# Kernel tuning notes

Hardware: AMD Instinct MI355X
Metric: run time of the kernel (lower is better)

## Reference

```python
import jax, jax.numpy as jnp
import numpy as np


def setup_inputs() -> dict:
    key = jax.random.key(0)
    k1, k2 = jax.random.split(key)
    N_rays, N_samples, NJ = 4096, 96, 24
    pts = jax.random.normal(k1, (N_rays, N_samples, 3), dtype=jnp.float32)
    skts = jax.random.normal(k2, (N_rays, NJ, 4, 4), dtype=jnp.float32)
    return {"pts": pts, "skts": skts}


def reference(pts, skts):
    # pts: [R, S, 3] -> homogeneous [R, S, 4]
    pts_h = jnp.concatenate([pts, jnp.ones(pts.shape[:-1] + (1,), dtype=pts.dtype)], axis=-1)
    # skts: [R, J, 4, 4]; fused equivalent of expand/transpose/matmul/permute:
    # out[r, s, j, a] = sum_b skts[r, j, a, b] * pts_h[r, s, b]
    out = jnp.einsum("rjab,rsb->rsja", skts, pts_h)
    return out[..., :3]
```

## Files before the change

### kernel.cpp

```cpp
#include <hip/hip_runtime.h>


constexpr int S_DIM = 96;
constexpr int J_DIM = 24;
constexpr int SKT_STRIDE = 17;
constexpr int BLOCK = 256;
constexpr int PAIRS = S_DIM * J_DIM;
constexpr int ITERS = PAIRS / BLOCK;

__global__ __launch_bounds__(BLOCK) void w2l_kernel(
    const float* __restrict__ pts,
    const float* __restrict__ skts,
    float* __restrict__ out) {

    const int r = blockIdx.x;
    const int tid = threadIdx.x;

    __shared__ float s_skt[J_DIM * SKT_STRIDE];
    __shared__ float s_pts[S_DIM * 3];

    const float* __restrict__ skt_g = skts + (size_t)r * (J_DIM * 16);
    const float* __restrict__ pts_g = pts  + (size_t)r * (S_DIM * 3);

    for (int i = tid; i < J_DIM * 16 + S_DIM * 3; i += BLOCK) {
        if (i < J_DIM * 16) {
            s_skt[(i >> 4) * SKT_STRIDE + (i & 15)] = skt_g[i];
        } else {
            int k = i - J_DIM * 16;
            s_pts[k] = pts_g[k];
        }
    }
    __syncthreads();

    float* __restrict__ out_r = out + (size_t)r * (PAIRS * 3);

    #pragma unroll
    for (int it = 0; it < ITERS; ++it) {
        const int p = tid + it * BLOCK;
        const int s = p / J_DIM;
        const int j = p - s * J_DIM;

        const float x = s_pts[s * 3 + 0];
        const float y = s_pts[s * 3 + 1];
        const float z = s_pts[s * 3 + 2];

        const float* __restrict__ b = &s_skt[j * SKT_STRIDE];
        const float o0 = fmaf(b[0], x, fmaf(b[1], y, fmaf(b[2],  z, b[3])));
        const float o1 = fmaf(b[4], x, fmaf(b[5], y, fmaf(b[6],  z, b[7])));
        const float o2 = fmaf(b[8], x, fmaf(b[9], y, fmaf(b[10], z, b[11])));

        *reinterpret_cast<float3*>(out_r + (size_t)p * 3) = make_float3(o0, o1, o2);
    }
}

extern "C" void kernel_launch(void* const* d_in, const int* in_sizes, int n_in,
                              void* d_out, int out_size, void* d_ws, size_t ws_size,
                              hipStream_t stream) {
    const float* pts  = (const float*)d_in[0];
    const float* skts = (const float*)d_in[1];
    float* out = (float*)d_out;

    const int R = in_sizes[0] / (S_DIM * 3);
    w2l_kernel<<<R, BLOCK, 0, stream>>>(pts, skts, out);
}
```

Measured before the change: 25.14 us.

## Process two rays per block with prefetched float4 loads into double-buffered LDS

Each block now handles two rays. While computing the first ray it prefetches the second ray's transforms and points into registers using float4 loads, then writes them into a second shared-memory buffer. This hides global load latency behind compute and stores, and uses vectorized loads in place of scalar ones. In exchange the grid is halved (2048 blocks), which reduces parallelism, and the launch assumes R is even.

```diff
diff --git a/kernel.cpp b/kernel.cpp
--- a/kernel.cpp
+++ b/kernel.cpp
@@ -3,53 +3,79 @@
 
 constexpr int S_DIM = 96;
 constexpr int J_DIM = 24;
-constexpr int SKT_STRIDE = 17;
+constexpr int STR   = 17;
 constexpr int BLOCK = 256;
 constexpr int PAIRS = S_DIM * J_DIM;
 constexpr int ITERS = PAIRS / BLOCK;
+constexpr int RPB   = 2;
+constexpr int SKT_F4 = J_DIM * 4;
+constexpr int PTS_F4 = S_DIM * 3 / 4;
+constexpr int TOT_F4 = SKT_F4 + PTS_F4;
 
 __global__ __launch_bounds__(BLOCK) void w2l_kernel(
     const float* __restrict__ pts,
     const float* __restrict__ skts,
     float* __restrict__ out) {
 
-    const int r = blockIdx.x;
     const int tid = threadIdx.x;
+    const int r0  = blockIdx.x * RPB;
 
-    __shared__ float s_skt[J_DIM * SKT_STRIDE];
-    __shared__ float s_pts[S_DIM * 3];
+    __shared__ float s_skt[RPB][J_DIM * STR];
+    __shared__ float s_pts[RPB][S_DIM * 3];
 
-    const float* __restrict__ skt_g = skts + (size_t)r * (J_DIM * 16);
-    const float* __restrict__ pts_g = pts  + (size_t)r * (S_DIM * 3);
+    auto load_ray = [&](int r, float4& v) {
+        if (tid < SKT_F4) {
+            v = reinterpret_cast<const float4*>(skts + (size_t)r * (J_DIM * 16))[tid];
+        } else if (tid < TOT_F4) {
+            v = reinterpret_cast<const float4*>(pts + (size_t)r * (S_DIM * 3))[tid - SKT_F4];
+        }
+    };
+    auto write_lds = [&](int buf, const float4& v) {
+        if (tid < SKT_F4) {
+            int row = tid >> 2, c = (tid & 3) * 4;
+            float* d = &s_skt[buf][row * STR + c];
+            d[0] = v.x; d[1] = v.y; d[2] = v.z; d[3] = v.w;
+        } else if (tid < TOT_F4) {
+            float* d = &s_pts[buf][(tid - SKT_F4) * 4];
+            d[0] = v.x; d[1] = v.y; d[2] = v.z; d[3] = v.w;
+        }
+    };
 
-    for (int i = tid; i < J_DIM * 16 + S_DIM * 3; i += BLOCK) {
-        if (i < J_DIM * 16) {
-            s_skt[(i >> 4) * SKT_STRIDE + (i & 15)] = skt_g[i];
-        } else {
-            int k = i - J_DIM * 16;
-            s_pts[k] = pts_g[k];
-        }
-    }
+    float4 v;
+    load_ray(r0, v);
+    write_lds(0, v);
     __syncthreads();
 
-    float* __restrict__ out_r = out + (size_t)r * (PAIRS * 3);
+    for (int rr = 0; rr < RPB; ++rr) {
+        float4 nv;
+        if (rr + 1 < RPB) load_ray(r0 + rr + 1, nv);
 
-    #pragma unroll
-    for (int it = 0; it < ITERS; ++it) {
-        const int p = tid + it * BLOCK;
-        const int s = p / J_DIM;
-        const int j = p - s * J_DIM;
+        float* __restrict__ out_r = out + (size_t)(r0 + rr) * (PAIRS * 3);
+        const float* __restrict__ sk = s_skt[rr];
+        const float* __restrict__ sp = s_pts[rr];
 
-        const float x = s_pts[s * 3 + 0];
-        const float y = s_pts[s * 3 + 1];
-        const float z = s_pts[s * 3 + 2];
+        #pragma unroll
+        for (int it = 0; it < ITERS; ++it) {
+            const int p = tid + it * BLOCK;
+            const int s = p / J_DIM;
+            const int j = p - s * J_DIM;
 
-        const float* __restrict__ b = &s_skt[j * SKT_STRIDE];
-        const float o0 = fmaf(b[0], x, fmaf(b[1], y, fmaf(b[2],  z, b[3])));
-        const float o1 = fmaf(b[4], x, fmaf(b[5], y, fmaf(b[6],  z, b[7])));
-        const float o2 = fmaf(b[8], x, fmaf(b[9], y, fmaf(b[10], z, b[11])));
+            const float x = sp[s * 3 + 0];
+            const float y = sp[s * 3 + 1];
+            const float z = sp[s * 3 + 2];
 
-        *reinterpret_cast<float3*>(out_r + (size_t)p * 3) = make_float3(o0, o1, o2);
+            const float* __restrict__ b = &sk[j * STR];
+            const float o0 = fmaf(b[0], x, fmaf(b[1], y, fmaf(b[2],  z, b[3])));
+            const float o1 = fmaf(b[4], x, fmaf(b[5], y, fmaf(b[6],  z, b[7])));
+            const float o2 = fmaf(b[8], x, fmaf(b[9], y, fmaf(b[10], z, b[11])));
+
+            *reinterpret_cast<float3*>(out_r + (size_t)p * 3) = make_float3(o0, o1, o2);
+        }
+
+        if (rr + 1 < RPB) {
+            write_lds(rr + 1, nv);
+            __syncthreads();
+        }
     }
 }
 
@@ -61,5 +87,5 @@
     float* out = (float*)d_out;
 
     const int R = in_sizes[0] / (S_DIM * 3);
-    w2l_kernel<<<R, BLOCK, 0, stream>>>(pts, skts, out);
+    w2l_kernel<<<R / RPB, BLOCK, 0, stream>>>(pts, skts, out);
 }
```

Result: faster. 23.92 us (-4.9%).

## Vectorize stores to float4, compute four joints per thread, two rays per block

Applied to the files above, without the earlier changes.

Each thread now computes 4 joints for one sample and writes 12 contiguous floats as three float4 stores, replacing the per-pair float3 stores. Shared memory holds points padded to float4 and skinning matrices at stride 20, so both are read with vector loads. Each 384-thread block processes two rays, which halves the grid size. The kernel is output-bandwidth bound, so the wider stores are meant to improve write efficiency, at the cost of a smaller grid and more registers per thread.

```diff
diff --git a/kernel.cpp b/kernel.cpp
--- a/kernel.cpp
+++ b/kernel.cpp
@@ -3,53 +3,76 @@
 
 constexpr int S_DIM = 96;
 constexpr int J_DIM = 24;
-constexpr int SKT_STRIDE = 17;
-constexpr int BLOCK = 256;
-constexpr int PAIRS = S_DIM * J_DIM;
-constexpr int ITERS = PAIRS / BLOCK;
+constexpr int BLOCK = 384;
+constexpr int RPB   = 2;
+constexpr int SKT_STR   = 20;
+constexpr int SKT_WORDS = J_DIM * SKT_STR;
+constexpr int PTS_WORDS = S_DIM * 4;
+constexpr int UNITS = RPB * S_DIM * J_DIM * 3 / 12;
+constexpr int ITERS = UNITS / BLOCK;
+constexpr int RAY_FLOATS = S_DIM * J_DIM * 3;
 
 __global__ __launch_bounds__(BLOCK) void w2l_kernel(
     const float* __restrict__ pts,
     const float* __restrict__ skts,
     float* __restrict__ out) {
 
-    const int r = blockIdx.x;
     const int tid = threadIdx.x;
+    const int r0  = blockIdx.x * RPB;
 
-    __shared__ float s_skt[J_DIM * SKT_STRIDE];
-    __shared__ float s_pts[S_DIM * 3];
+    __shared__ __align__(16) float s_skt[RPB][SKT_WORDS];
+    __shared__ __align__(16) float s_pts[RPB][PTS_WORDS];
 
-    const float* __restrict__ skt_g = skts + (size_t)r * (J_DIM * 16);
-    const float* __restrict__ pts_g = pts  + (size_t)r * (S_DIM * 3);
+    const float* __restrict__ skt_g = skts + (size_t)r0 * (J_DIM * 16);
+    const float* __restrict__ pts_g = pts  + (size_t)r0 * (S_DIM * 3);
 
-    for (int i = tid; i < J_DIM * 16 + S_DIM * 3; i += BLOCK) {
-        if (i < J_DIM * 16) {
-            s_skt[(i >> 4) * SKT_STRIDE + (i & 15)] = skt_g[i];
-        } else {
-            int k = i - J_DIM * 16;
-            s_pts[k] = pts_g[k];
-        }
+    if (tid < RPB * 96) {
+        float4 v = reinterpret_cast<const float4*>(skt_g)[tid];
+        int ray = tid / 96, g = tid - ray * 96;
+        int j = g >> 2, a = g & 3;
+        *reinterpret_cast<float4*>(&s_skt[ray][j * SKT_STR + a * 4]) = v;
+        int s = tid % S_DIM, ray2 = tid / S_DIM;
+        s_pts[ray2][s * 4 + 3] = 1.0f;
+    }
+    #pragma unroll
+    for (int q = tid; q < RPB * S_DIM * 3; q += BLOCK) {
+        float v = pts_g[q];
+        int ray = q / (S_DIM * 3), qq = q - ray * (S_DIM * 3);
+        int s = qq / 3, c = qq - s * 3;
+        s_pts[ray][s * 4 + c] = v;
     }
     __syncthreads();
 
-    float* __restrict__ out_r = out + (size_t)r * (PAIRS * 3);
+    float* __restrict__ out_p = out + (size_t)r0 * RAY_FLOATS;
 
     #pragma unroll
     for (int it = 0; it < ITERS; ++it) {
-        const int p = tid + it * BLOCK;
-        const int s = p / J_DIM;
-        const int j = p - s * J_DIM;
+        const int u   = tid + it * BLOCK;
+        const int ray = u / 576;
+        const int up  = u - ray * 576;
+        const int s   = up / 6;
+        const int jstart = (up - s * 6) * 4;
 
-        const float x = s_pts[s * 3 + 0];
-        const float y = s_pts[s * 3 + 1];
-        const float z = s_pts[s * 3 + 2];
+        const float4 P = *reinterpret_cast<const float4*>(&s_pts[ray][s * 4]);
+        const float* __restrict__ base = &s_skt[ray][jstart * SKT_STR];
 
-        const float* __restrict__ b = &s_skt[j * SKT_STRIDE];
-        const float o0 = fmaf(b[0], x, fmaf(b[1], y, fmaf(b[2],  z, b[3])));
-        const float o1 = fmaf(b[4], x, fmaf(b[5], y, fmaf(b[6],  z, b[7])));
-        const float o2 = fmaf(b[8], x, fmaf(b[9], y, fmaf(b[10], z, b[11])));
+        float o12[12];
+        #pragma unroll
+        for (int jj = 0; jj < 4; ++jj) {
+            const float4 B0 = *reinterpret_cast<const float4*>(base + jj * SKT_STR + 0);
+            const float4 B1 = *reinterpret_cast<const float4*>(base + jj * SKT_STR + 4);
+            const float4 B2 = *reinterpret_cast<const float4*>(base + jj * SKT_STR + 8);
+            o12[jj * 3 + 0] = fmaf(B0.x, P.x, fmaf(B0.y, P.y, fmaf(B0.z, P.z, B0.w)));
+            o12[jj * 3 + 1] = fmaf(B1.x, P.x, fmaf(B1.y, P.y, fmaf(B1.z, P.z, B1.w)));
+            o12[jj * 3 + 2] = fmaf(B2.x, P.x, fmaf(B2.y, P.y, fmaf(B2.z, P.z, B2.w)));
+        }
 
-        *reinterpret_cast<float3*>(out_r + (size_t)p * 3) = make_float3(o0, o1, o2);
+        float* __restrict__ dst = out_p + (size_t)u * 12;
+        #pragma unroll
+        for (int k = 0; k < 3; ++k) {
+            *reinterpret_cast<float4*>(dst + 4 * k) =
+                make_float4(o12[4 * k], o12[4 * k + 1], o12[4 * k + 2], o12[4 * k + 3]);
+        }
     }
 }
 
@@ -61,5 +84,5 @@
     float* out = (float*)d_out;
 
     const int R = in_sizes[0] / (S_DIM * 3);
-    w2l_kernel<<<R, BLOCK, 0, stream>>>(pts, skts, out);
+    w2l_kernel<<<R / RPB, BLOCK, 0, stream>>>(pts, skts, out);
 }
```

Measured after the change: 35.11 us. 39.7% more time.

## Process two rays per block with double-buffered LDS and register-held transforms

Applied to the files above, without the earlier changes.

Each block now handles two rays with 384 threads. Every thread keeps its joint's 3x4 transform in registers and reads padded float4 points from LDS. The next ray's inputs are prefetched into registers while the current ray computes, then written to the other LDS buffer. This cuts per-pair LDS loads and integer division, and overlaps global loads with compute. In exchange it halves the grid size, which may reduce latency hiding, and assumes R is even.

```diff
diff --git a/kernel.cpp b/kernel.cpp
--- a/kernel.cpp
+++ b/kernel.cpp
@@ -3,53 +3,80 @@
 
 constexpr int S_DIM = 96;
 constexpr int J_DIM = 24;
-constexpr int SKT_STRIDE = 17;
-constexpr int BLOCK = 256;
-constexpr int PAIRS = S_DIM * J_DIM;
-constexpr int ITERS = PAIRS / BLOCK;
+constexpr int BLOCK = 384;
+constexpr int RPB   = 2;
+constexpr int SKT_STR   = 20;
+constexpr int SKT_WORDS = J_DIM * SKT_STR;
+constexpr int PTS_WORDS = S_DIM * 4;
+constexpr int ITERS = S_DIM * J_DIM / BLOCK;
+constexpr int RAY_FLOATS = S_DIM * J_DIM * 3;
 
 __global__ __launch_bounds__(BLOCK) void w2l_kernel(
     const float* __restrict__ pts,
     const float* __restrict__ skts,
     float* __restrict__ out) {
 
-    const int r = blockIdx.x;
     const int tid = threadIdx.x;
+    const int r0  = blockIdx.x * RPB;
 
-    __shared__ float s_skt[J_DIM * SKT_STRIDE];
-    __shared__ float s_pts[S_DIM * 3];
+    __shared__ __align__(16) float s_skt[2][SKT_WORDS];
+    __shared__ __align__(16) float s_pts[2][PTS_WORDS];
 
-    const float* __restrict__ skt_g = skts + (size_t)r * (J_DIM * 16);
-    const float* __restrict__ pts_g = pts  + (size_t)r * (S_DIM * 3);
+    const int s0 = tid / J_DIM;
+    const int j  = tid - s0 * J_DIM;
 
-    for (int i = tid; i < J_DIM * 16 + S_DIM * 3; i += BLOCK) {
-        if (i < J_DIM * 16) {
-            s_skt[(i >> 4) * SKT_STRIDE + (i & 15)] = skt_g[i];
+    auto load_ray = [&](int r, float4& v, float& pv) {
+        if (tid < 96) {
+            v = reinterpret_cast<const float4*>(skts + (size_t)r * (J_DIM * 16))[tid];
         } else {
-            int k = i - J_DIM * 16;
-            s_pts[k] = pts_g[k];
+            pv = pts[(size_t)r * (S_DIM * 3) + (tid - 96)];
         }
-    }
+    };
+    auto write_lds = [&](int buf, const float4& v, float pv) {
+        if (tid < 96) {
+            int jj = tid >> 2, a = tid & 3;
+            *reinterpret_cast<float4*>(&s_skt[buf][jj * SKT_STR + a * 4]) = v;
+            s_pts[buf][tid * 4 + 3] = 1.0f;
+        } else {
+            int q = tid - 96;
+            int sq = q / 3, c = q - 3 * sq;
+            s_pts[buf][sq * 4 + c] = pv;
+        }
+    };
+
+    float4 v; float pv;
+    load_ray(r0, v, pv);
+    write_lds(0, v, pv);
     __syncthreads();
 
-    float* __restrict__ out_r = out + (size_t)r * (PAIRS * 3);
+    for (int rr = 0; rr < RPB; ++rr) {
+        const int cur = rr & 1;
+        float4 nv; float npv;
+        if (rr + 1 < RPB) load_ray(r0 + rr + 1, nv, npv);
 
-    #pragma unroll
-    for (int it = 0; it < ITERS; ++it) {
-        const int p = tid + it * BLOCK;
-        const int s = p / J_DIM;
-        const int j = p - s * J_DIM;
+        const float4 B0 = *reinterpret_cast<const float4*>(&s_skt[cur][j * SKT_STR + 0]);
+        const float4 B1 = *reinterpret_cast<const float4*>(&s_skt[cur][j * SKT_STR + 4]);
+        const float4 B2 = *reinterpret_cast<const float4*>(&s_skt[cur][j * SKT_STR + 8]);
 
-        const float x = s_pts[s * 3 + 0];
-        const float y = s_pts[s * 3 + 1];
-        const float z = s_pts[s * 3 + 2];
+        float* __restrict__ out_r = out + (size_t)(r0 + rr) * RAY_FLOATS;
 
-        const float* __restrict__ b = &s_skt[j * SKT_STRIDE];
-        const float o0 = fmaf(b[0], x, fmaf(b[1], y, fmaf(b[2],  z, b[3])));
-        const float o1 = fmaf(b[4], x, fmaf(b[5], y, fmaf(b[6],  z, b[7])));
-        const float o2 = fmaf(b[8], x, fmaf(b[9], y, fmaf(b[10], z, b[11])));
+        #pragma unroll
+        for (int it = 0; it < ITERS; ++it) {
+            const int s = s0 + it * 16;
+            const float4 P = *reinterpret_cast<const float4*>(&s_pts[cur][s * 4]);
 
-        *reinterpret_cast<float3*>(out_r + (size_t)p * 3) = make_float3(o0, o1, o2);
+            const float ox = fmaf(B0.x, P.x, fmaf(B0.y, P.y, fmaf(B0.z, P.z, B0.w)));
+            const float oy = fmaf(B1.x, P.x, fmaf(B1.y, P.y, fmaf(B1.z, P.z, B1.w)));
+            const float oz = fmaf(B2.x, P.x, fmaf(B2.y, P.y, fmaf(B2.z, P.z, B2.w)));
+
+            const int p = tid + it * BLOCK;
+            *reinterpret_cast<float3*>(out_r + (size_t)p * 3) = make_float3(ox, oy, oz);
+        }
+
+        if (rr + 1 < RPB) {
+            write_lds(cur ^ 1, nv, npv);
+            __syncthreads();
+        }
     }
 }
 
@@ -61,5 +88,5 @@
     float* out = (float*)d_out;
 
     const int R = in_sizes[0] / (S_DIM * 3);
-    w2l_kernel<<<R, BLOCK, 0, stream>>>(pts, skts, out);
+    w2l_kernel<<<R / RPB, BLOCK, 0, stream>>>(pts, skts, out);
 }
```

Measured after the change: 24.20 us. -3.7%, faster.
